# Optimization experiments

Hardware: AMD Instinct MI355X
Metric: run time of the kernel (lower is better)

Reference implementation:

```python
import jax, jax.numpy as jnp
import numpy as np

DIM = 1024; H = 16; DH = 64; L = 32; W = 8; E = 4  # ext_len = window_size//2
SEQ = 4096; B = 4
LN_EPS = 1e-5


def _ln(x, g, b):
    m = x.mean(-1, keepdims=True)
    v = ((x - m) ** 2).mean(-1, keepdims=True)
    return (x - m) / jnp.sqrt(v + LN_EPS) * g + b


def _split(x):  # (b,s,H*dh) -> (b,H,s,dh)
    b, s, _ = x.shape
    return x.reshape(b, s, H, DH).transpose(0, 2, 1, 3)


def _forward(query, Wq, bq, Wk, bk, Wv, bv, Wo, bo, g_l, b_l, g_s, b_s, Wd, bd):
    X = query.transpose(1, 0, 2)  # (b,s,d); s already multiple of W so no pad
    b, s, _ = X.shape
    Q = _split(X @ Wq + bq) * (1.0 / np.sqrt(DH))           # (b,H,s,dh)
    K = _split(_ln(X @ Wk + bk, g_l, b_l))
    V = _split(_ln(X @ Wv + bv, g_l, b_l))

    # landmark compression: softmax over sequence dim (no padding -> no mask)
    head_scores = jax.nn.softmax(X @ Wd + bd, axis=1)       # (b,s,H*L)
    hs = head_scores.reshape(b, s, H, L).transpose(0, 2, 3, 1)  # (b,H,L,s)
    Kc = jnp.einsum('bhls,bhsd->bhld', hs, K)
    Vc = jnp.einsum('bhls,bhsd->bhld', hs, V)
    # dual_ln_s applied over the flattened head dim, per landmark
    Kc = _split(_ln(Kc.transpose(0, 2, 1, 3).reshape(b, L, DIM), g_s, b_s))
    Vc = _split(_ln(Vc.transpose(0, 2, 1, 3).reshape(b, L, DIM), g_s, b_s))

    attn_compress = jnp.einsum('bhsd,bhld->bhsl', Q, Kc)    # (b,H,s,L)

    # sliding window band (v2): pad E on each side, tile into groups of W
    g = s // W
    band = W + 2 * E  # 16
    idx = jnp.arange(g)[:, None] * W + jnp.arange(band)[None, :]  # (g,band)
    K_pad = jnp.pad(K, ((0, 0), (0, 0), (E, E), (0, 0)))
    K_tiles = K_pad[:, :, idx, :]                           # (b,H,g,band,dh)
    Q_tiles = Q.reshape(b, H, g, W, DH)
    win = jnp.einsum('bhgwd,bhgkd->bhgwk', Q_tiles, K_tiles)
    valid = jnp.pad(jnp.ones((s,), bool), (E, E))[idx]      # (g,band) halo=False
    win = jnp.where(valid[None, None, :, None, :], win, -jnp.inf)
    win_flat = win.reshape(b, H, s, band)

    all_attn = jax.nn.softmax(jnp.concatenate([attn_compress, win_flat], -1), axis=-1)
    C = jnp.einsum('bhsl,bhld->bhsd', all_attn[..., :L], Vc)
    win_probs = all_attn[..., L:].reshape(b, H, g, W, band)
    V_pad = jnp.pad(V, ((0, 0), (0, 0), (E, E), (0, 0)))
    V_tiles = V_pad[:, :, idx, :]
    C = C + jnp.einsum('bhgwk,bhgkd->bhgwd', win_probs, V_tiles).reshape(b, H, s, DH)

    out = C.transpose(0, 2, 1, 3).reshape(b, s, DIM) @ Wo + bo
    return out.transpose(1, 0, 2)  # (s,b,d)


def setup_inputs() -> dict:
    key = jax.random.key(0)
    ks = jax.random.split(key, 7)
    sc = 0.02
    return {
        'query': jax.random.normal(ks[0], (SEQ, B, DIM), jnp.float32),
        'Wq': jax.random.normal(ks[1], (DIM, DIM), jnp.float32) * sc,
        'bq': jnp.zeros((DIM,), jnp.float32),
        'Wk': jax.random.normal(ks[2], (DIM, DIM), jnp.float32) * sc,
        'bk': jnp.zeros((DIM,), jnp.float32),
        'Wv': jax.random.normal(ks[3], (DIM, DIM), jnp.float32) * sc,
        'bv': jnp.zeros((DIM,), jnp.float32),
        'Wo': jax.random.normal(ks[4], (DIM, DIM), jnp.float32) * sc,
        'bo': jnp.zeros((DIM,), jnp.float32),
        'g_l': jnp.ones((DIM,), jnp.float32),
        'b_l': jnp.zeros((DIM,), jnp.float32),
        'g_s': jnp.ones((DIM,), jnp.float32),
        'b_s': jnp.zeros((DIM,), jnp.float32),
        'Wd': jax.random.normal(ks[5], (DIM, H * L), jnp.float32) * sc,
        'bd': jnp.zeros((H * L,), jnp.float32),
    }


def reference(query, Wq, bq, Wk, bk, Wv, bv, Wo, bo, g_l, b_l, g_s, b_s, Wd, bd):
    return _forward(query, Wq, bq, Wk, bk, Wv, bv, Wo, bo, g_l, b_l, g_s, b_s, Wd, bd)
```

## Files before the change

kernel.cpp:

```cpp
#include <hip/hip_runtime.h>
#include <cstddef>
#include <cstdint>

#define DIMC 1024
#define HC   16
#define DHC  64
#define LC   32
#define WC   8
#define EC   4
#define SEQC 4096
#define BC   4
#define MTOT 16384

typedef __attribute__((ext_vector_type(8))) __bf16 bf16x8;
typedef __attribute__((ext_vector_type(4))) float f32x4;

__device__ inline unsigned short f2b(float f) {
  unsigned int u = __float_as_uint(f);
  u += 0x7fff + ((u >> 16) & 1);
  return (unsigned short)(u >> 16);
}
__device__ inline float b2f(unsigned short u) {
  return __uint_as_float(((unsigned int)u) << 16);
}

__device__ inline void gll16(const void* g, void* l) {
  __builtin_amdgcn_global_load_lds(
      (__attribute__((address_space(1))) void*)g,
      (__attribute__((address_space(3))) void*)l, 16, 0, 0);
}

__global__ __launch_bounds__(256) void conv_rows(const float* __restrict__ src,
    unsigned short* __restrict__ dst) {
  int r = blockIdx.x;
  int sr = ((r & 4095) << 2) | (r >> 12);
  const float4* s = (const float4*)(src + (size_t)sr * 1024);
  ushort4* d = (ushort4*)(dst + (size_t)r * 1024);
  int t = threadIdx.x;
  float4 v = s[t];
  d[t] = make_ushort4(f2b(v.x), f2b(v.y), f2b(v.z), f2b(v.w));
}

__global__ __launch_bounds__(256) void conv_wT_all(
    const float* __restrict__ Wq, const float* __restrict__ Wk,
    const float* __restrict__ Wv, const float* __restrict__ Wd,
    const float* __restrict__ Wo, unsigned short* __restrict__ wAll,
    unsigned short* __restrict__ woT) {
  __shared__ float tile[32][33];
  int z = blockIdx.z;
  const float* W = (z == 0) ? Wq : (z == 1) ? Wk : (z == 2) ? Wv
                   : (z == 3) ? Wd : Wo;
  unsigned short* WT = (z == 4) ? woT : (wAll + (size_t)z * 1048576);
  int N = (z == 3) ? 512 : 1024;
  int n0 = blockIdx.x * 32, k0 = blockIdx.y * 32;
  if (n0 >= N) return;
  int t = threadIdx.x;
  int tr = t >> 5, tc = t & 31;
#pragma unroll
  for (int i = 0; i < 4; ++i)
    tile[tr + i * 8][tc] = W[(size_t)(k0 + tr + i * 8) * N + n0 + tc];
  __syncthreads();
#pragma unroll
  for (int i = 0; i < 4; ++i)
    WT[(size_t)(n0 + tr + i * 8) * 1024 + k0 + tc] = f2b(tile[tc][tr + i * 8]);
}

__global__ __launch_bounds__(512, 2) void gemm256(
    const unsigned short* __restrict__ A, const unsigned short* __restrict__ BT,
    const float* __restrict__ b0, const float* __restrict__ b1,
    const float* __restrict__ b2, const float* __restrict__ b3,
    unsigned short* __restrict__ o0, unsigned short* __restrict__ o1,
    unsigned short* __restrict__ o2, float* __restrict__ oy,
    float* __restrict__ outf, int mode) {
  extern __shared__ char smb[];
  unsigned short* smu = (unsigned short*)smb;
  int t = threadIdx.x;
  int w = t >> 6, lane = t & 63;
  int m = lane & 15, q4 = lane >> 4;
  int wr = (w >> 2) * 128, wc = (w & 3) * 64;
  int id = blockIdx.x;
  int xcd = id & 7, jj0 = id >> 3;
  int rowT = xcd * 8 + (jj0 & 7), colT = jj0 >> 3;
  int rowBase = rowT * 256, nBase = colT * 256;

  int srow = t >> 3;
  int colSwz = (((t & 7) ^ (srow & 7)) << 3);
  const unsigned short* gA[4];
  const unsigned short* gB[4];
  int ldsOff[4];
#pragma unroll
  for (int q = 0; q < 4; ++q) {
    int rof = (q >> 1) * 128 + (q & 1) * 64 + srow;
    gA[q] = A + (size_t)(rowBase + rof) * 1024 + colSwz;
    gB[q] = BT + (size_t)(nBase + rof) * 1024 + colSwz;
    ldsOff[q] = q * 8192 + w * 1024;
  }
  int gx0 = ((q4) ^ (m & 7)) << 3;
  int gx1 = ((4 + q4) ^ (m & 7)) << 3;
  f32x4 acc[8][4] = {};

#pragma unroll
  for (int q = 0; q < 4; ++q) {
    gll16(gA[q], smb + ldsOff[q]);
    gll16(gB[q], smb + 65536 + ldsOff[q]);
  }
#pragma unroll
  for (int q = 0; q < 4; ++q) {
    gll16(gA[q] + 64, smb + 32768 + ldsOff[q]);
    gll16(gB[q] + 64, smb + 65536 + 32768 + ldsOff[q]);
  }
  asm volatile("s_waitcnt vmcnt(8)" ::: "memory");
  __builtin_amdgcn_s_barrier();
  __builtin_amdgcn_sched_barrier(0);

  for (int kt = 0; kt < 16; ++kt) {
    int c = kt & 1;
    const unsigned short* Au = smu + c * 16384;
    const unsigned short* Bu = smu + 32768 + c * 16384;
    bf16x8 bf[4][2];
#pragma unroll
    for (int jj = 0; jj < 4; ++jj) {
      int rb = (wc + jj * 16 + m) * 64;
      bf[jj][0] = *(const bf16x8*)(Bu + rb + gx0);
      bf[jj][1] = *(const bf16x8*)(Bu + rb + gx1);
    }
#pragma unroll
    for (int ip = 0; ip < 4; ++ip) {
      bf16x8 af[2][2];
#pragma unroll
      for (int i2 = 0; i2 < 2; ++i2) {
        int ra = (wr + (ip * 2 + i2) * 16 + m) * 64;
        af[i2][0] = *(const bf16x8*)(Au + ra + gx0);
        af[i2][1] = *(const bf16x8*)(Au + ra + gx1);
      }
      __builtin_amdgcn_s_setprio(1);
#pragma unroll
      for (int i2 = 0; i2 < 2; ++i2)
#pragma unroll
        for (int jj = 0; jj < 4; ++jj) {
          acc[ip * 2 + i2][jj] = __builtin_amdgcn_mfma_f32_16x16x32_bf16(
              af[i2][0], bf[jj][0], acc[ip * 2 + i2][jj], 0, 0, 0);
          acc[ip * 2 + i2][jj] = __builtin_amdgcn_mfma_f32_16x16x32_bf16(
              af[i2][1], bf[jj][1], acc[ip * 2 + i2][jj], 0, 0, 0);
        }
      __builtin_amdgcn_s_setprio(0);
    }
    if (kt == 15) break;
    __builtin_amdgcn_s_barrier();
    if (kt < 14) {
      int kc = (kt + 2) * 64;
#pragma unroll
      for (int q = 0; q < 4; ++q) {
        gll16(gA[q] + kc, smb + c * 32768 + ldsOff[q]);
        gll16(gB[q] + kc, smb + 65536 + c * 32768 + ldsOff[q]);
      }
      asm volatile("s_waitcnt vmcnt(8)" ::: "memory");
    } else {
      asm volatile("s_waitcnt vmcnt(0)" ::: "memory");
    }
    __builtin_amdgcn_s_barrier();
    __builtin_amdgcn_sched_barrier(0);
  }
  __syncthreads();

  int segBase = nBase + wc;
  if (mode == 1) {
#pragma unroll
    for (int jj = 0; jj < 4; ++jj) {
      float bvv = b0[segBase + jj * 16 + m];
#pragma unroll
      for (int i = 0; i < 8; ++i)
#pragma unroll
        for (int r = 0; r < 4; ++r) {
          int rr = rowBase + wr + i * 16 + q4 * 4 + r;
          int orow = ((rr & 4095) << 2) | (rr >> 12);
          outf[(size_t)orow * 1024 + segBase + jj * 16 + m] =
              acc[i][jj][r] + bvv;
        }
    }
    return;
  }
  int seg = segBase >> 10;
  if (seg == 3) {
    int lc = segBase - 3072;
#pragma unroll
    for (int jj = 0; jj < 4; ++jj) {
      float bvv = b3[lc + jj * 16 + m];
#pragma unroll
      for (int i = 0; i < 8; ++i)
#pragma unroll
        for (int r = 0; r < 4; ++r)
          oy[(size_t)(rowBase + wr + i * 16 + q4 * 4 + r) * 512 + lc +
             jj * 16 + m] = acc[i][jj][r] + bvv;
    }
    return;
  }
  const float* bp = (seg == 0) ? b0 : (seg == 1) ? b1 : b2;
  unsigned short* ob = (seg == 0) ? o0 : (seg == 1) ? o1 : o2;
  float scl = (seg == 0) ? 0.125f : 1.0f;
#pragma unroll
  for (int jj = 0; jj < 4; ++jj) {
    float bvv = bp[(segBase & 1023) + jj * 16 + m];
#pragma unroll
    for (int i = 0; i < 8; ++i)
#pragma unroll
      for (int r = 0; r < 4; ++r)
        smu[(wr + i * 16 + q4 * 4 + r) * 264 + wc + jj * 16 + m] =
            f2b((acc[i][jj][r] + bvv) * scl);
  }
  __syncthreads();
  int lc0 = nBase & 1023;
#pragma unroll
  for (int rd = 0; rd < 16; ++rd) {
    int idx = rd * 512 + t;
    int row = idx >> 5, cs = (idx & 31) * 8;
    uint4 v = *(const uint4*)(smu + row * 264 + cs);
    *(uint4*)(ob + (size_t)(rowBase + row) * 1024 + lc0 + cs) = v;
  }
}

__global__ __launch_bounds__(256) void ln_bf(unsigned short* __restrict__ buf,
    const float* __restrict__ g, const float* __restrict__ b) {
  int row = blockIdx.x;
  unsigned short* p = buf + (size_t)row * 1024;
  int tid = threadIdx.x;
  ushort4 u4 = ((const ushort4*)p)[tid];
  float x0 = b2f(u4.x), x1 = b2f(u4.y), x2 = b2f(u4.z), x3 = b2f(u4.w);
  float s = x0 + x1 + x2 + x3;
  float ss = x0 * x0 + x1 * x1 + x2 * x2 + x3 * x3;
#pragma unroll
  for (int off = 32; off > 0; off >>= 1) {
    s += __shfl_down(s, off);
    ss += __shfl_down(ss, off);
  }
  __shared__ float sred[8], ssred[8];
  int wave = tid >> 6, lane = tid & 63;
  if (lane == 0) { sred[wave] = s; ssred[wave] = ss; }
  __syncthreads();
  if (tid == 0) {
    float S = 0, SS = 0;
    for (int w = 0; w < 4; ++w) { S += sred[w]; SS += ssred[w]; }
    float m = S * (1.0f / 1024.0f);
    float v = SS * (1.0f / 1024.0f) - m * m;
    sred[0] = m;
    ssred[0] = rsqrtf(v + 1e-5f);
  }
  __syncthreads();
  float m = sred[0], rinv = ssred[0];
  float4 gg = ((const float4*)g)[tid];
  float4 bb = ((const float4*)b)[tid];
  ushort4 y;
  y.x = f2b((x0 - m) * rinv * gg.x + bb.x);
  y.y = f2b((x1 - m) * rinv * gg.y + bb.y);
  y.z = f2b((x2 - m) * rinv * gg.z + bb.z);
  y.w = f2b((x3 - m) * rinv * gg.w + bb.w);
  ((ushort4*)p)[tid] = y;
}

__global__ __launch_bounds__(256) void col_part(const float* __restrict__ yd,
    float* __restrict__ pm, float* __restrict__ ps) {
  int cg = blockIdx.x, b = blockIdx.y, sc = blockIdx.z;
  int t = threadIdx.x;
  int lane = t & 63, grp = t >> 6;
  const float* base = yd + (size_t)b * 4096 * 512 + (size_t)(sc * 256) * 512 +
                      cg * 64 + lane;
  float m = -1e30f, s = 0.f;
  for (int r = grp; r < 256; r += 4) {
    float x = base[(size_t)r * 512];
    float mn = fmaxf(m, x);
    s = s * expf(m - mn) + expf(x - mn);
    m = mn;
  }
  __shared__ float mS[4][64], sS[4][64];
  mS[grp][lane] = m;
  sS[grp][lane] = s;
  __syncthreads();
  if (grp == 0) {
    float M = mS[0][lane], S = sS[0][lane];
#pragma unroll
    for (int k = 1; k < 4; ++k) {
      float m2 = mS[k][lane], s2 = sS[k][lane];
      float Mn = fmaxf(M, m2);
      S = S * expf(M - Mn) + s2 * expf(m2 - Mn);
      M = Mn;
    }
    int col = cg * 64 + lane;
    pm[((size_t)(b * 512 + col)) * 16 + sc] = M;
    ps[((size_t)(b * 512 + col)) * 16 + sc] = S;
  }
}

__global__ __launch_bounds__(256) void col_combine(const float* __restrict__ pm,
    const float* __restrict__ ps, float* __restrict__ stats) {
  int idx = blockIdx.x * 256 + threadIdx.x;
  float M = -1e30f, S = 0.f;
#pragma unroll
  for (int sc = 0; sc < 16; ++sc) {
    float m2 = pm[(size_t)idx * 16 + sc], s2 = ps[(size_t)idx * 16 + sc];
    float Mn = fmaxf(M, m2);
    S = S * expf(M - Mn) + s2 * expf(m2 - Mn);
    M = Mn;
  }
  stats[(size_t)idx * 2] = M;
  stats[(size_t)idx * 2 + 1] = 1.0f / S;
}

#define NCHUNK 32
#define SCH    128
__global__ __launch_bounds__(256) void compress(const float* __restrict__ yd,
    const float* __restrict__ stats, const unsigned short* __restrict__ kbuf,
    const unsigned short* __restrict__ vbuf, float* __restrict__ kcp,
    float* __restrict__ vcp) {
  int c = blockIdx.x, h = blockIdx.y, b = blockIdx.z;
  int tid = threadIdx.x;
  int dq = tid & 15;
  int lp = tid >> 4;
  __shared__ float mxS[32], isS[32];
  __shared__ float pS[16][32];
  __shared__ float KfS[16][64];
  __shared__ float VfS[16][64];
  if (tid < 32) {
    mxS[tid] = stats[(size_t)(b * 512 + h * 32 + tid) * 2];
    isS[tid] = stats[(size_t)(b * 512 + h * 32 + tid) * 2 + 1];
  }
  __syncthreads();
  f32x4 aK0 = {}, aK1 = {}, aV0 = {}, aV1 = {};
  int s0 = c * SCH;
  for (int sc = 0; sc < SCH; sc += 16) {
    int bs = b * 4096 + s0 + sc;
    {
      int sl = tid >> 4;
      int l2 = (tid & 15) * 2;
      const float2 yv =
          *(const float2*)(yd + ((size_t)(bs + sl)) * 512 + h * 32 + l2);
      pS[sl][l2] = expf(yv.x - mxS[l2]) * isS[l2];
      pS[sl][l2 + 1] = expf(yv.y - mxS[l2 + 1]) * isS[l2 + 1];
      size_t roff = ((size_t)(bs + sl)) * 1024 + h * 64 + (tid & 15) * 4;
      ushort4 ku = *(const ushort4*)(kbuf + roff);
      ushort4 vu = *(const ushort4*)(vbuf + roff);
      f32x4 kf, vf;
      kf[0] = b2f(ku.x); kf[1] = b2f(ku.y); kf[2] = b2f(ku.z); kf[3] = b2f(ku.w);
      vf[0] = b2f(vu.x); vf[1] = b2f(vu.y); vf[2] = b2f(vu.z); vf[3] = b2f(vu.w);
      *(f32x4*)&KfS[sl][(tid & 15) * 4] = kf;
      *(f32x4*)&VfS[sl][(tid & 15) * 4] = vf;
    }
    __syncthreads();
#pragma unroll
    for (int sl = 0; sl < 16; ++sl) {
      float p0 = pS[sl][lp * 2];
      float p1 = pS[sl][lp * 2 + 1];
      const f32x4 kk = *(const f32x4*)&KfS[sl][dq * 4];
      const f32x4 vv = *(const f32x4*)&VfS[sl][dq * 4];
#pragma unroll
      for (int q = 0; q < 4; ++q) {
        aK0[q] += p0 * kk[q];
        aK1[q] += p1 * kk[q];
        aV0[q] += p0 * vv[q];
        aV1[q] += p1 * vv[q];
      }
    }
    __syncthreads();
  }
  size_t o0 = ((((size_t)c * 4 + b) * 16 + h) * 32 + (lp * 2)) * 64 + dq * 4;
  *(f32x4*)&kcp[o0] = aK0;
  *(f32x4*)&kcp[o0 + 64] = aK1;
  *(f32x4*)&vcp[o0] = aV0;
  *(f32x4*)&vcp[o0 + 64] = aV1;
}

__global__ __launch_bounds__(256) void ln_compress(const float* __restrict__ kcp,
    const float* __restrict__ vcp, const float* __restrict__ g_s,
    const float* __restrict__ b_s, float* __restrict__ kc_ln,
    float* __restrict__ vc_ln) {
  int row = blockIdx.x;
  int b = row >> 5, l = row & 31;
  const float* part = blockIdx.y ? vcp : kcp;
  float* outp = blockIdx.y ? vc_ln : kc_ln;
  int tid = threadIdx.x;
  int h = tid >> 4, d4 = (tid & 15) * 4;
  size_t base = (((size_t)b * 16 + h) * 32 + l) * 64 + d4;
  f32x4 x = {};
#pragma unroll
  for (int cch = 0; cch < NCHUNK; ++cch) {
    const f32x4 v = *(const f32x4*)&part[base + (size_t)cch * 131072];
#pragma unroll
    for (int q = 0; q < 4; ++q) x[q] += v[q];
  }
  float lsum = x[0] + x[1] + x[2] + x[3];
  float lss = x[0] * x[0] + x[1] * x[1] + x[2] * x[2] + x[3] * x[3];
#pragma unroll
  for (int off = 32; off > 0; off >>= 1) {
    lsum += __shfl_down(lsum, off);
    lss += __shfl_down(lss, off);
  }
  __shared__ float red[8], red2[8];
  int wave = tid >> 6, lane = tid & 63;
  if (lane == 0) { red[wave] = lsum; red2[wave] = lss; }
  __syncthreads();
  if (tid == 0) {
    float S = 0, SS = 0;
    for (int w = 0; w < 4; ++w) { S += red[w]; SS += red2[w]; }
    float m = S * (1.0f / 1024.0f);
    float v = SS * (1.0f / 1024.0f) - m * m;
    red[0] = m;
    red2[0] = rsqrtf(v + 1e-5f);
  }
  __syncthreads();
  float m = red[0], rinv = red2[0];
  int j = tid * 4;
  const float4 gg = *(const float4*)(g_s + j);
  const float4 bb = *(const float4*)(b_s + j);
  float4 yo;
  yo.x = (x[0] - m) * rinv * gg.x + bb.x;
  yo.y = (x[1] - m) * rinv * gg.y + bb.y;
  yo.z = (x[2] - m) * rinv * gg.z + bb.z;
  yo.w = (x[3] - m) * rinv * gg.w + bb.w;
  *(float4*)(outp + (size_t)row * 1024 + j) = yo;
}

__global__ __launch_bounds__(256) void attention(unsigned short* __restrict__ qc,
    const unsigned short* __restrict__ kbuf,
    const unsigned short* __restrict__ vbuf,
    const float* __restrict__ kc_ln, const float* __restrict__ vc_ln) {
  int qt = blockIdx.x, h = blockIdx.y, b = blockIdx.z;
  int t = threadIdx.x;
  int l = t & 63, w = t >> 6;
  int lr16 = l & 15, q4 = l >> 4;
  int s0 = qt * 64, hoff = h * 64;

  __shared__ unsigned short regionA[12672];
  __shared__ unsigned short Vt[64 * 128];
  unsigned short* Qs = regionA;
  unsigned short* Ks = regionA + 64 * 72;
  unsigned short* Ps = regionA;
  unsigned short* Cs = regionA + 64 * 128;

#pragma unroll
  for (int it = 0; it < 2; ++it) {
    int sid = it * 256 + t;
    int row = sid >> 3, seg = sid & 7;
    uint4 v = *(const uint4*)(qc + ((size_t)(b * 4096 + s0 + row)) * 1024 +
                              hoff + seg * 8);
    *(uint4*)(Qs + row * 72 + seg * 8) = v;
  }
#pragma unroll
  for (int it = 0; it < 2; ++it) {
    int sid = it * 256 + t;
    int row = sid >> 4, s4 = sid & 15;
    float4 v = *(const float4*)(kc_ln + ((size_t)(b * 32 + row)) * 1024 +
                                hoff + s4 * 4);
    ushort4 u = make_ushort4(f2b(v.x), f2b(v.y), f2b(v.z), f2b(v.w));
    *(ushort4*)(Ks + row * 72 + s4 * 4) = u;
  }
#pragma unroll
  for (int it = 0; it < 3; ++it) {
    int sid = it * 256 + t;
    if (sid < 576) {
      int r = sid >> 3, seg = sid & 7;
      int pos = s0 - 4 + r;
      uint4 v = {0, 0, 0, 0};
      if (pos >= 0 && pos < 4096)
        v = *(const uint4*)(kbuf + ((size_t)(b * 4096 + pos)) * 1024 + hoff +
                            seg * 8);
      *(uint4*)(Ks + (32 + r) * 72 + seg * 8) = v;
    }
  }
#pragma unroll
  for (int it = 0; it < 8; ++it) {
    int d = t & 63;
    int k0 = (t >> 6) * 4 + it * 16;
    unsigned short vv[4];
#pragma unroll
    for (int i = 0; i < 4; ++i) {
      int kk = k0 + i;
      unsigned short x = 0;
      if (kk < 32) {
        x = f2b(vc_ln[((size_t)(b * 32 + kk)) * 1024 + hoff + d]);
      } else if (kk < 104) {
        int pos = s0 - 4 + (kk - 32);
        if (pos >= 0 && pos < 4096)
          x = vbuf[((size_t)(b * 4096 + pos)) * 1024 + hoff + d];
      }
      vv[i] = x;
    }
    *(ushort4*)(Vt + d * 128 + (k0 ^ ((d & 31) << 2))) = *(ushort4*)vv;
  }
  __syncthreads();

  int mbase = w * 16;
  bf16x8 aq[2];
#pragma unroll
  for (int ks = 0; ks < 2; ++ks)
    aq[ks] = *(const bf16x8*)(Qs + (mbase + lr16) * 72 + ks * 32 + q4 * 8);
  f32x4 S[7];
#pragma unroll
  for (int nb = 0; nb < 7; ++nb) {
    f32x4 acc = {};
#pragma unroll
    for (int ks = 0; ks < 2; ++ks) {
      bf16x8 bk =
          *(const bf16x8*)(Ks + (nb * 16 + lr16) * 72 + ks * 32 + q4 * 8);
      acc = __builtin_amdgcn_mfma_f32_16x16x32_bf16(aq[ks], bk, acc, 0, 0, 0);
    }
    S[nb] = acc;
  }

  float ex[7][4];
#pragma unroll
  for (int r = 0; r < 4; ++r) {
    int qrow = mbase + q4 * 4 + r;
    int g8 = (qrow >> 3) * 8;
    float m = -1e30f;
#pragma unroll
    for (int nb = 0; nb < 7; ++nb) {
      int col = nb * 16 + lr16;
      float v = S[nb][r];
      if (col >= 32) {
        int rw = col - 32;
        int pos = s0 - 4 + rw;
        bool ok = (rw >= g8) && (rw < g8 + 16) && (pos >= 0) && (pos < 4096);
        if (!ok) v = -INFINITY;
      }
      ex[nb][r] = v;
      m = fmaxf(m, v);
    }
    m = fmaxf(m, __shfl_xor(m, 1));
    m = fmaxf(m, __shfl_xor(m, 2));
    m = fmaxf(m, __shfl_xor(m, 4));
    m = fmaxf(m, __shfl_xor(m, 8));
    float s = 0.f;
#pragma unroll
    for (int nb = 0; nb < 7; ++nb) {
      float e = expf(ex[nb][r] - m);
      ex[nb][r] = e;
      s += e;
    }
    s += __shfl_xor(s, 1);
    s += __shfl_xor(s, 2);
    s += __shfl_xor(s, 4);
    s += __shfl_xor(s, 8);
    float inv = 1.0f / s;
#pragma unroll
    for (int nb = 0; nb < 7; ++nb) ex[nb][r] *= inv;
  }
  __syncthreads();

  if (t < 128) {
    int q = t >> 1, blk = 14 + (t & 1);
    uint4 z = {0, 0, 0, 0};
    *(uint4*)(Ps + q * 128 + ((blk ^ (q & 7)) << 3)) = z;
  }
#pragma unroll
  for (int r = 0; r < 4; ++r) {
    int q = mbase + q4 * 4 + r;
#pragma unroll
    for (int nb = 0; nb < 7; ++nb) {
      int col = nb * 16 + lr16;
      int blk = col >> 3;
      Ps[q * 128 + ((blk ^ (q & 7)) << 3) + (col & 7)] = f2b(ex[nb][r]);
    }
  }
  __syncthreads();

  bf16x8 pa[4];
#pragma unroll
  for (int ks = 0; ks < 4; ++ks) {
    int q = mbase + lr16;
    int blk = ks * 4 + q4;
    pa[ks] = *(const bf16x8*)(Ps + q * 128 + ((blk ^ (q & 7)) << 3));
  }
#pragma unroll
  for (int nb = 0; nb < 4; ++nb) {
    f32x4 acc = {};
    int d = nb * 16 + lr16;
#pragma unroll
    for (int ks = 0; ks < 4; ++ks) {
      unsigned short vv[8];
#pragma unroll
      for (int jh = 0; jh < 2; ++jh) {
        int k4 = ks * 32 + q4 * 8 + jh * 4;
        *(ushort4*)(vv + jh * 4) =
            *(const ushort4*)(Vt + d * 128 + (k4 ^ ((d & 31) << 2)));
      }
      acc = __builtin_amdgcn_mfma_f32_16x16x32_bf16(pa[ks], *(const bf16x8*)vv,
                                                    acc, 0, 0, 0);
    }
#pragma unroll
    for (int r = 0; r < 4; ++r) {
      int row = mbase + q4 * 4 + r;
      Cs[row * 68 + d] = f2b(acc[r]);
    }
  }
  __syncthreads();

#pragma unroll
  for (int it = 0; it < 2; ++it) {
    int sid = it * 256 + t;
    int row = sid >> 3, seg = sid & 7;
    ushort4 a0 = *(const ushort4*)(Cs + row * 68 + seg * 8);
    ushort4 a1 = *(const ushort4*)(Cs + row * 68 + seg * 8 + 4);
    unsigned short u[8];
    *(ushort4*)u = a0;
    *(ushort4*)(u + 4) = a1;
    *(uint4*)(qc + ((size_t)(b * 4096 + s0 + row)) * 1024 + hoff + seg * 8) =
        *(uint4*)u;
  }
}

extern "C" void kernel_launch(void* const* d_in, const int* in_sizes, int n_in,
                              void* d_out, int out_size, void* d_ws,
                              size_t ws_size, hipStream_t stream) {
  const float* query = (const float*)d_in[0];
  const float* Wq = (const float*)d_in[1];
  const float* bq = (const float*)d_in[2];
  const float* Wk = (const float*)d_in[3];
  const float* bk = (const float*)d_in[4];
  const float* Wv = (const float*)d_in[5];
  const float* bv = (const float*)d_in[6];
  const float* Wo = (const float*)d_in[7];
  const float* bo = (const float*)d_in[8];
  const float* g_l = (const float*)d_in[9];
  const float* b_l = (const float*)d_in[10];
  const float* g_s = (const float*)d_in[11];
  const float* b_s = (const float*)d_in[12];
  const float* Wd = (const float*)d_in[13];
  const float* bd = (const float*)d_in[14];
  float* out = (float*)d_out;

  static bool attr_set = []() {
    hipFuncSetAttribute((const void*)gemm256,
                        hipFuncAttributeMaxDynamicSharedMemorySize, 135168);
    return true;
  }();
  (void)attr_set;

  unsigned short* qb = (unsigned short*)d_ws;
  unsigned short* kb = qb + 16777216;
  unsigned short* vb = kb + 16777216;
  unsigned short* xb = vb + 16777216;
  float* yd = (float*)(xb + 16777216);
  float* stats = yd + 8388608;
  float* col_pm = stats + 4096;
  float* col_ps = col_pm + 32768;
  float* kc_part = col_ps + 32768;
  float* vc_part = kc_part + 4194304;
  float* kc_ln = vc_part + 4194304;
  float* vc_ln = kc_ln + 131072;
  unsigned short* wAll = (unsigned short*)(vc_ln + 131072);
  unsigned short* woT = wAll + 3670016;

  dim3 blk(256);
  conv_rows<<<16384, blk, 0, stream>>>(query, xb);
  conv_wT_all<<<dim3(32, 32, 5), blk, 0, stream>>>(Wq, Wk, Wv, Wd, Wo,
                                                   wAll, woT);
  gemm256<<<896, dim3(512), 135168, stream>>>(xb, wAll, bq, bk, bv, bd,
                                              qb, kb, vb, yd, nullptr, 0);
  ln_bf<<<32768, blk, 0, stream>>>(kb, g_l, b_l);
  col_part<<<dim3(8, 4, 16), blk, 0, stream>>>(yd, col_pm, col_ps);
  col_combine<<<8, blk, 0, stream>>>(col_pm, col_ps, stats);
  compress<<<dim3(NCHUNK, 16, 4), blk, 0, stream>>>(yd, stats, kb, vb,
                                                    kc_part, vc_part);
  ln_compress<<<dim3(128, 2), blk, 0, stream>>>(kc_part, vc_part, g_s, b_s,
                                                kc_ln, vc_ln);
  attention<<<dim3(64, 16, 4), blk, 0, stream>>>(qb, kb, vb, kc_ln, vc_ln);
  gemm256<<<256, dim3(512), 135168, stream>>>(qb, woT, bo, nullptr, nullptr,
                                              nullptr, nullptr, nullptr,
                                              nullptr, nullptr, out, 1);
}
```

Measured before the change: 509.5 us.

## Halve GEMM K-tile to 32 and split epilogue staging to cut LDS

The 256x256 GEMM now stages K-slices of 32 instead of 64 per double-buffered step, with a new XOR swizzle and twice as many loop iterations. The bf16 output epilogue is staged through shared memory in two 128-row halves, so dynamic LDS drops from 135168 to 67584 bytes. The goal is to let two 512-thread blocks fit per CU, matching the launch bounds, and gain latency hiding. The cost is more barriers per K step and less MFMA work between syncs.

```diff
diff --git a/kernel.cpp b/kernel.cpp
--- a/kernel.cpp
+++ b/kernel.cpp
@@ -83,78 +83,61 @@
   int rowT = xcd * 8 + (jj0 & 7), colT = jj0 >> 3;
   int rowBase = rowT * 256, nBase = colT * 256;
 
-  int srow = t >> 3;
-  int colSwz = (((t & 7) ^ (srow & 7)) << 3);
-  const unsigned short* gA[4];
-  const unsigned short* gB[4];
-  int ldsOff[4];
-#pragma unroll
-  for (int q = 0; q < 4; ++q) {
-    int rof = (q >> 1) * 128 + (q & 1) * 64 + srow;
-    gA[q] = A + (size_t)(rowBase + rof) * 1024 + colSwz;
-    gB[q] = BT + (size_t)(nBase + rof) * 1024 + colSwz;
-    ldsOff[q] = q * 8192 + w * 1024;
-  }
-  int gx0 = ((q4) ^ (m & 7)) << 3;
-  int gx1 = ((4 + q4) ^ (m & 7)) << 3;
+  int srow = t >> 2;
+  int gsw = ((t & 3) ^ ((t >> 3) & 3)) * 8;
+  const unsigned short* gA0 = A + (size_t)(rowBase + srow) * 1024 + gsw;
+  const unsigned short* gA1 = A + (size_t)(rowBase + 128 + srow) * 1024 + gsw;
+  const unsigned short* gB0 = BT + (size_t)(nBase + srow) * 1024 + gsw;
+  const unsigned short* gB1 = BT + (size_t)(nBase + 128 + srow) * 1024 + gsw;
+  int ldsP0 = w * 1024;
+  int ldsP1 = 8192 + w * 1024;
+  int sx = (q4 ^ ((m >> 1) & 3)) * 8;
   f32x4 acc[8][4] = {};
 
-#pragma unroll
-  for (int q = 0; q < 4; ++q) {
-    gll16(gA[q], smb + ldsOff[q]);
-    gll16(gB[q], smb + 65536 + ldsOff[q]);
-  }
-#pragma unroll
-  for (int q = 0; q < 4; ++q) {
-    gll16(gA[q] + 64, smb + 32768 + ldsOff[q]);
-    gll16(gB[q] + 64, smb + 65536 + 32768 + ldsOff[q]);
-  }
-  asm volatile("s_waitcnt vmcnt(8)" ::: "memory");
+#define STAGE5(kt_, c_)                                              \
+  {                                                                  \
+    int kc_ = (kt_) * 32;                                            \
+    gll16(gA0 + kc_, smb + (c_)*16384 + ldsP0);                      \
+    gll16(gA1 + kc_, smb + (c_)*16384 + ldsP1);                      \
+    gll16(gB0 + kc_, smb + 32768 + (c_)*16384 + ldsP0);              \
+    gll16(gB1 + kc_, smb + 32768 + (c_)*16384 + ldsP1);              \
+  }
+
+  STAGE5(0, 0);
+  STAGE5(1, 1);
+  asm volatile("s_waitcnt vmcnt(4)" ::: "memory");
   __builtin_amdgcn_s_barrier();
   __builtin_amdgcn_sched_barrier(0);
 
-  for (int kt = 0; kt < 16; ++kt) {
+  for (int kt = 0; kt < 32; ++kt) {
     int c = kt & 1;
-    const unsigned short* Au = smu + c * 16384;
-    const unsigned short* Bu = smu + 32768 + c * 16384;
-    bf16x8 bf[4][2];
-#pragma unroll
-    for (int jj = 0; jj < 4; ++jj) {
-      int rb = (wc + jj * 16 + m) * 64;
-      bf[jj][0] = *(const bf16x8*)(Bu + rb + gx0);
-      bf[jj][1] = *(const bf16x8*)(Bu + rb + gx1);
-    }
+    const unsigned short* Au = smu + c * 8192;
+    const unsigned short* Bu = smu + 16384 + c * 8192;
+    bf16x8 bf[4];
+#pragma unroll
+    for (int jj = 0; jj < 4; ++jj)
+      bf[jj] = *(const bf16x8*)(Bu + (wc + jj * 16 + m) * 32 + sx);
 #pragma unroll
     for (int ip = 0; ip < 4; ++ip) {
-      bf16x8 af[2][2];
-#pragma unroll
-      for (int i2 = 0; i2 < 2; ++i2) {
-        int ra = (wr + (ip * 2 + i2) * 16 + m) * 64;
-        af[i2][0] = *(const bf16x8*)(Au + ra + gx0);
-        af[i2][1] = *(const bf16x8*)(Au + ra + gx1);
-      }
+      bf16x8 af0 = *(const bf16x8*)(Au + (wr + (ip * 2) * 16 + m) * 32 + sx);
+      bf16x8 af1 =
+          *(const bf16x8*)(Au + (wr + (ip * 2 + 1) * 16 + m) * 32 + sx);
       __builtin_amdgcn_s_setprio(1);
 #pragma unroll
-      for (int i2 = 0; i2 < 2; ++i2)
-#pragma unroll
-        for (int jj = 0; jj < 4; ++jj) {
-          acc[ip * 2 + i2][jj] = __builtin_amdgcn_mfma_f32_16x16x32_bf16(
-              af[i2][0], bf[jj][0], acc[ip * 2 + i2][jj], 0, 0, 0);
-          acc[ip * 2 + i2][jj] = __builtin_amdgcn_mfma_f32_16x16x32_bf16(
-              af[i2][1], bf[jj][1], acc[ip * 2 + i2][jj], 0, 0, 0);
-        }
+      for (int jj = 0; jj < 4; ++jj)
+        acc[ip * 2][jj] = __builtin_amdgcn_mfma_f32_16x16x32_bf16(
+            af0, bf[jj], acc[ip * 2][jj], 0, 0, 0);
+#pragma unroll
+      for (int jj = 0; jj < 4; ++jj)
+        acc[ip * 2 + 1][jj] = __builtin_amdgcn_mfma_f32_16x16x32_bf16(
+            af1, bf[jj], acc[ip * 2 + 1][jj], 0, 0, 0);
       __builtin_amdgcn_s_setprio(0);
     }
-    if (kt == 15) break;
+    if (kt == 31) break;
     __builtin_amdgcn_s_barrier();
-    if (kt < 14) {
-      int kc = (kt + 2) * 64;
-#pragma unroll
-      for (int q = 0; q < 4; ++q) {
-        gll16(gA[q] + kc, smb + c * 32768 + ldsOff[q]);
-        gll16(gB[q] + kc, smb + 65536 + c * 32768 + ldsOff[q]);
-      }
-      asm volatile("s_waitcnt vmcnt(8)" ::: "memory");
+    if (kt < 30) {
+      STAGE5(kt + 2, c);
+      asm volatile("s_waitcnt vmcnt(4)" ::: "memory");
     } else {
       asm volatile("s_waitcnt vmcnt(0)" ::: "memory");
     }
@@ -198,24 +181,30 @@
   const float* bp = (seg == 0) ? b0 : (seg == 1) ? b1 : b2;
   unsigned short* ob = (seg == 0) ? o0 : (seg == 1) ? o1 : o2;
   float scl = (seg == 0) ? 0.125f : 1.0f;
-#pragma unroll
-  for (int jj = 0; jj < 4; ++jj) {
-    float bvv = bp[(segBase & 1023) + jj * 16 + m];
-#pragma unroll
-    for (int i = 0; i < 8; ++i)
-#pragma unroll
-      for (int r = 0; r < 4; ++r)
-        smu[(wr + i * 16 + q4 * 4 + r) * 264 + wc + jj * 16 + m] =
-            f2b((acc[i][jj][r] + bvv) * scl);
-  }
-  __syncthreads();
   int lc0 = nBase & 1023;
 #pragma unroll
-  for (int rd = 0; rd < 16; ++rd) {
-    int idx = rd * 512 + t;
-    int row = idx >> 5, cs = (idx & 31) * 8;
-    uint4 v = *(const uint4*)(smu + row * 264 + cs);
-    *(uint4*)(ob + (size_t)(rowBase + row) * 1024 + lc0 + cs) = v;
+  for (int h = 0; h < 2; ++h) {
+    if ((w >> 2) == h) {
+#pragma unroll
+      for (int jj = 0; jj < 4; ++jj) {
+        float bvv = bp[lc0 + wc + jj * 16 + m];
+#pragma unroll
+        for (int i = 0; i < 8; ++i)
+#pragma unroll
+          for (int r = 0; r < 4; ++r)
+            smu[(i * 16 + q4 * 4 + r) * 264 + wc + jj * 16 + m] =
+                f2b((acc[i][jj][r] + bvv) * scl);
+      }
+    }
+    __syncthreads();
+#pragma unroll
+    for (int rd = 0; rd < 8; ++rd) {
+      int idx = rd * 512 + t;
+      int row = idx >> 5, cs = (idx & 31) * 8;
+      uint4 v = *(const uint4*)(smu + row * 264 + cs);
+      *(uint4*)(ob + (size_t)(rowBase + h * 128 + row) * 1024 + lc0 + cs) = v;
+    }
+    __syncthreads();
   }
 }
 
@@ -653,8 +642,8 @@
   conv_rows<<<16384, blk, 0, stream>>>(query, xb);
   conv_wT_all<<<dim3(32, 32, 5), blk, 0, stream>>>(Wq, Wk, Wv, Wd, Wo,
                                                    wAll, woT);
-  gemm256<<<896, dim3(512), 135168, stream>>>(xb, wAll, bq, bk, bv, bd,
-                                              qb, kb, vb, yd, nullptr, 0);
+  gemm256<<<896, dim3(512), 67584, stream>>>(xb, wAll, bq, bk, bv, bd,
+                                             qb, kb, vb, yd, nullptr, 0);
   ln_bf<<<32768, blk, 0, stream>>>(kb, g_l, b_l);
   col_part<<<dim3(8, 4, 16), blk, 0, stream>>>(yd, col_pm, col_ps);
   col_combine<<<8, blk, 0, stream>>>(col_pm, col_ps, stats);
@@ -663,7 +652,7 @@
   ln_compress<<<dim3(128, 2), blk, 0, stream>>>(kc_part, vc_part, g_s, b_s,
                                                 kc_ln, vc_ln);
   attention<<<dim3(64, 16, 4), blk, 0, stream>>>(qb, kb, vb, kc_ln, vc_ln);
-  gemm256<<<256, dim3(512), 135168, stream>>>(qb, woT, bo, nullptr, nullptr,
-                                              nullptr, nullptr, nullptr,
-                                              nullptr, nullptr, out, 1);
-}
+  gemm256<<<256, dim3(512), 67584, stream>>>(qb, woT, bo, nullptr, nullptr,
+                                             nullptr, nullptr, nullptr,
+                                             nullptr, nullptr, out, 1);
+}
```

New measurement: 521.7 us. 1.02x slower.
